# Optimization experiments

Measured on AMD Instinct MI355X. Metric: run time of the kernel, lower is better.

Reference implementation:

```python
import jax, jax.numpy as jnp
import numpy as np

EPS = 1e-8

def setup_inputs() -> dict:
    key = jax.random.key(0)
    k1, k2 = jax.random.split(key)
    B, C, H, W = 8, 21, 512, 512
    inp = jax.random.normal(k1, (B, C, H, W), dtype=jnp.float32)
    target = jax.random.uniform(k2, (B, C, H, W), dtype=jnp.float32)
    return {"input": inp, "target": target}

def reference(input, target):
    B, C, H, W = input.shape
    # argmax over class dim -> [B, H, W]
    pred = jnp.argmax(input, axis=1)
    # one-hot of prediction, flattened over spatial dims -> [B, HW, C]
    h = jax.nn.one_hot(pred.reshape(B, H * W), C, dtype=input.dtype)
    # target flattened over spatial dims -> [B, C, HW]
    y = target.reshape(B, C, H * W)
    # cm[b, i, j] = sum_n y[b, i, n] * h[b, n, j]  -> [B, C, C]
    cm = jnp.einsum('bin,bnj->bij', y, h)
    # row-normalize by target mass per class, then mean over batch -> [C, C]
    cm = cm / (jnp.sum(y, axis=2, keepdims=True) + EPS)
    return jnp.mean(cm, axis=0)
```

## Files before the change

kernel.cpp:

```cpp
#include <hip/hip_runtime.h>

#define NC 21
#define NB 8
#define HW (512*512)
#define EPS 1e-8f
#define NREP 8
#define NTILE 256
#define PSTRIDE 512

typedef float f32x4 __attribute__((ext_vector_type(4)));


template <bool PARTIAL>
__global__ __launch_bounds__(256) void cm_accum(const float* __restrict__ input,
                                                const float* __restrict__ target,
                                                float* __restrict__ cm ,
                                                float* __restrict__ partial ) {
    __shared__ float scm[NREP][NC * NC];
    const int t = threadIdx.x;
    for (int i = t; i < NREP * NC * NC; i += 256) ((float*)scm)[i] = 0.0f;
    __syncthreads();

    const int b    = blockIdx.x >> 8;
    const int tile = blockIdx.x & 255;
    const int q    = (tile << 8) + t;

    const f32x4* ip = (const f32x4*)(input  + (size_t)b * NC * HW);
    const f32x4* tp = (const f32x4*)(target + (size_t)b * NC * HW);
    const int plane4 = HW / 4;

    f32x4 v[NC];
    #pragma unroll
    for (int c = 0; c < NC; ++c) v[c] = __builtin_nontemporal_load(ip + c * plane4 + q);
    __builtin_amdgcn_sched_barrier(0);

    f32x4 m = v[0];
    int jx = 0, jy = 0, jz = 0, jw = 0;
    #pragma unroll
    for (int c = 1; c < NC; ++c) {
        if (v[c].x > m.x) { m.x = v[c].x; jx = c; }
        if (v[c].y > m.y) { m.y = v[c].y; jy = c; }
        if (v[c].z > m.z) { m.z = v[c].z; jz = c; }
        if (v[c].w > m.w) { m.w = v[c].w; jw = c; }
    }

    f32x4 y[NC];
    #pragma unroll
    for (int c = 0; c < NC; ++c) y[c] = __builtin_nontemporal_load(tp + c * plane4 + q);
    __builtin_amdgcn_sched_barrier(0);

    float* my = scm[t & (NREP - 1)];
    #pragma unroll
    for (int c = 0; c < NC; ++c) {
        const int row = c * NC;
        atomicAdd(&my[row + jx], y[c].x);
        atomicAdd(&my[row + jy], y[c].y);
        atomicAdd(&my[row + jz], y[c].z);
        atomicAdd(&my[row + jw], y[c].w);
    }
    __syncthreads();

    if (PARTIAL) {
        float* pout = partial + (size_t)blockIdx.x * PSTRIDE;
        for (int i = t; i < PSTRIDE; i += 256) {
            float s = 0.0f;
            if (i < NC * NC) {
                #pragma unroll
                for (int r = 0; r < NREP; ++r) s += scm[r][i];
            }
            pout[i] = s;
        }
    } else {
        for (int i = t; i < NC * NC; i += 256) {
            float s = 0.0f;
            #pragma unroll
            for (int r = 0; r < NREP; ++r) s += scm[r][i];
            atomicAdd(&cm[b * NC * NC + i], s);
        }
    }
}

__global__ __launch_bounds__(256) void cm_reduce(const float* __restrict__ partial,
                                                 float* __restrict__ cm) {
    const int b = blockIdx.x, t = threadIdx.x;
    const float* p = partial + (size_t)b * NTILE * PSTRIDE;
    float s0 = 0.0f, s1 = 0.0f;
    #pragma unroll 8
    for (int s = 0; s < NTILE; ++s) {
        s0 += p[(size_t)s * PSTRIDE + t];
        s1 += p[(size_t)s * PSTRIDE + t + 256];
    }
    cm[b * NC * NC + t] = s0;
    if (t + 256 < NC * NC) cm[b * NC * NC + t + 256] = s1;
}

__global__ __launch_bounds__(512) void cm_final(const float* __restrict__ cm,
                                                float* __restrict__ out) {
    __shared__ float rs[NB * NC];
    const int t = threadIdx.x;
    if (t < NB * NC) {
        const int b = t / NC, i = t % NC;
        float s = 0.0f;
        for (int j = 0; j < NC; ++j) s += cm[b * NC * NC + i * NC + j];
        rs[t] = s + EPS;
    }
    __syncthreads();
    if (t < NC * NC) {
        const int i = t / NC;
        float acc = 0.0f;
        for (int b = 0; b < NB; ++b) acc += cm[b * NC * NC + t] / rs[b * NC + i];
        out[t] = acc * (1.0f / NB);
    }
}

extern "C" void kernel_launch(void* const* d_in, const int* in_sizes, int n_in,
                              void* d_out, int out_size, void* d_ws, size_t ws_size,
                              hipStream_t stream) {
    const float* input  = (const float*)d_in[0];
    const float* target = (const float*)d_in[1];
    float* out = (float*)d_out;

    const size_t partial_floats = (size_t)NB * NTILE * PSTRIDE;
    const size_t need = (partial_floats + NB * NC * NC) * sizeof(float);

    if (ws_size >= need) {
        float* partial = (float*)d_ws;
        float* cm      = partial + partial_floats;
        cm_accum<true><<<NB * NTILE, 256, 0, stream>>>(input, target, cm, partial);
        cm_reduce<<<NB, 256, 0, stream>>>(partial, cm);
        cm_final<<<1, 512, 0, stream>>>(cm, out);
    } else {
        float* cm = (float*)d_ws;
        hipMemsetAsync(cm, 0, NB * NC * NC * sizeof(float), stream);
        cm_accum<false><<<NB * NTILE, 256, 0, stream>>>(input, target, cm, nullptr);
        cm_final<<<1, 512, 0, stream>>>(cm, out);
    }
}
```

Before: 514.8 us.

## Stream class planes with double-buffered loads, two float4 per thread, rotated start channel

```diff
diff --git a/kernel.cpp b/kernel.cpp
--- a/kernel.cpp
+++ b/kernel.cpp
@@ -1,68 +1,97 @@
 #include <hip/hip_runtime.h>
+#include <math.h>
 
 #define NC 21
 #define NB 8
 #define HW (512*512)
 #define EPS 1e-8f
 #define NREP 8
-#define NTILE 256
+#define TPB 256
+#define G4 2
+#define F4_PER_BLOCK (TPB * G4)
+#define TILES_PER_IMG (HW / 4 / F4_PER_BLOCK)
+#define NBLK (NB * TILES_PER_IMG)
 #define PSTRIDE 512
 
 typedef float f32x4 __attribute__((ext_vector_type(4)));
 
 
+#define UPD(val, cc, mm, jj) \
+    if ((val) > (mm) || ((val) == (mm) && (cc) < (jj))) { (mm) = (val); (jj) = (cc); }
+
 template <bool PARTIAL>
-__global__ __launch_bounds__(256) void cm_accum(const float* __restrict__ input,
+__global__ __launch_bounds__(TPB) void cm_accum(const float* __restrict__ input,
                                                 const float* __restrict__ target,
                                                 float* __restrict__ cm ,
                                                 float* __restrict__ partial ) {
     __shared__ float scm[NREP][NC * NC];
     const int t = threadIdx.x;
-    for (int i = t; i < NREP * NC * NC; i += 256) ((float*)scm)[i] = 0.0f;
+    for (int i = t; i < NREP * NC * NC; i += TPB) ((float*)scm)[i] = 0.0f;
     __syncthreads();
 
-    const int b    = blockIdx.x >> 8;
-    const int tile = blockIdx.x & 255;
-    const int q    = (tile << 8) + t;
+    const int bid  = blockIdx.x;
+    const int b    = bid / TILES_PER_IMG;
+    const int tile = bid % TILES_PER_IMG;
+    const int rot  = bid % NC;
 
     const f32x4* ip = (const f32x4*)(input  + (size_t)b * NC * HW);
     const f32x4* tp = (const f32x4*)(target + (size_t)b * NC * HW);
     const int plane4 = HW / 4;
+    const int q0 = tile * F4_PER_BLOCK + t;
 
-    f32x4 v[NC];
-    #pragma unroll
-    for (int c = 0; c < NC; ++c) v[c] = __builtin_nontemporal_load(ip + c * plane4 + q);
-    __builtin_amdgcn_sched_barrier(0);
+    f32x4 mA, mB;
+    mA.x = mA.y = mA.z = mA.w = -INFINITY;
+    mB.x = mB.y = mB.z = mB.w = -INFINITY;
+    int jAx = NC, jAy = NC, jAz = NC, jAw = NC;
+    int jBx = NC, jBy = NC, jBz = NC, jBw = NC;
 
-    f32x4 m = v[0];
-    int jx = 0, jy = 0, jz = 0, jw = 0;
-    #pragma unroll
-    for (int c = 1; c < NC; ++c) {
-        if (v[c].x > m.x) { m.x = v[c].x; jx = c; }
-        if (v[c].y > m.y) { m.y = v[c].y; jy = c; }
-        if (v[c].z > m.z) { m.z = v[c].z; jz = c; }
-        if (v[c].w > m.w) { m.w = v[c].w; jw = c; }
+    int c = rot;
+    f32x4 curA = __builtin_nontemporal_load(ip + (size_t)c * plane4 + q0);
+    f32x4 curB = __builtin_nontemporal_load(ip + (size_t)c * plane4 + q0 + TPB);
+    f32x4 nxtA = {}, nxtB = {};
+    for (int cc = 0; cc < NC; ++cc) {
+        const int cn = (c + 1 == NC) ? 0 : c + 1;
+        if (cc < NC - 1) {
+            nxtA = __builtin_nontemporal_load(ip + (size_t)cn * plane4 + q0);
+            nxtB = __builtin_nontemporal_load(ip + (size_t)cn * plane4 + q0 + TPB);
+        }
+        __builtin_amdgcn_sched_barrier(0);
+        UPD(curA.x, c, mA.x, jAx); UPD(curA.y, c, mA.y, jAy);
+        UPD(curA.z, c, mA.z, jAz); UPD(curA.w, c, mA.w, jAw);
+        UPD(curB.x, c, mB.x, jBx); UPD(curB.y, c, mB.y, jBy);
+        UPD(curB.z, c, mB.z, jBz); UPD(curB.w, c, mB.w, jBw);
+        curA = nxtA; curB = nxtB;
+        c = cn;
     }
 
-    f32x4 y[NC];
-    #pragma unroll
-    for (int c = 0; c < NC; ++c) y[c] = __builtin_nontemporal_load(tp + c * plane4 + q);
-    __builtin_amdgcn_sched_barrier(0);
-
     float* my = scm[t & (NREP - 1)];
-    #pragma unroll
-    for (int c = 0; c < NC; ++c) {
+    c = rot;
+    curA = __builtin_nontemporal_load(tp + (size_t)c * plane4 + q0);
+    curB = __builtin_nontemporal_load(tp + (size_t)c * plane4 + q0 + TPB);
+    for (int cc = 0; cc < NC; ++cc) {
+        const int cn = (c + 1 == NC) ? 0 : c + 1;
+        if (cc < NC - 1) {
+            nxtA = __builtin_nontemporal_load(tp + (size_t)cn * plane4 + q0);
+            nxtB = __builtin_nontemporal_load(tp + (size_t)cn * plane4 + q0 + TPB);
+        }
+        __builtin_amdgcn_sched_barrier(0);
         const int row = c * NC;
-        atomicAdd(&my[row + jx], y[c].x);
-        atomicAdd(&my[row + jy], y[c].y);
-        atomicAdd(&my[row + jz], y[c].z);
-        atomicAdd(&my[row + jw], y[c].w);
+        atomicAdd(&my[row + jAx], curA.x);
+        atomicAdd(&my[row + jAy], curA.y);
+        atomicAdd(&my[row + jAz], curA.z);
+        atomicAdd(&my[row + jAw], curA.w);
+        atomicAdd(&my[row + jBx], curB.x);
+        atomicAdd(&my[row + jBy], curB.y);
+        atomicAdd(&my[row + jBz], curB.z);
+        atomicAdd(&my[row + jBw], curB.w);
+        curA = nxtA; curB = nxtB;
+        c = cn;
     }
     __syncthreads();
 
     if (PARTIAL) {
-        float* pout = partial + (size_t)blockIdx.x * PSTRIDE;
-        for (int i = t; i < PSTRIDE; i += 256) {
+        float* pout = partial + (size_t)bid * PSTRIDE;
+        for (int i = t; i < PSTRIDE; i += TPB) {
             float s = 0.0f;
             if (i < NC * NC) {
                 #pragma unroll
@@ -71,7 +100,7 @@
             pout[i] = s;
         }
     } else {
-        for (int i = t; i < NC * NC; i += 256) {
+        for (int i = t; i < NC * NC; i += TPB) {
             float s = 0.0f;
             #pragma unroll
             for (int r = 0; r < NREP; ++r) s += scm[r][i];
@@ -83,10 +112,10 @@
 __global__ __launch_bounds__(256) void cm_reduce(const float* __restrict__ partial,
                                                  float* __restrict__ cm) {
     const int b = blockIdx.x, t = threadIdx.x;
-    const float* p = partial + (size_t)b * NTILE * PSTRIDE;
+    const float* p = partial + (size_t)b * TILES_PER_IMG * PSTRIDE;
     float s0 = 0.0f, s1 = 0.0f;
     #pragma unroll 8
-    for (int s = 0; s < NTILE; ++s) {
+    for (int s = 0; s < TILES_PER_IMG; ++s) {
         s0 += p[(size_t)s * PSTRIDE + t];
         s1 += p[(size_t)s * PSTRIDE + t + 256];
     }
@@ -120,19 +149,19 @@
     const float* target = (const float*)d_in[1];
     float* out = (float*)d_out;
 
-    const size_t partial_floats = (size_t)NB * NTILE * PSTRIDE;
+    const size_t partial_floats = (size_t)NBLK * PSTRIDE;
     const size_t need = (partial_floats + NB * NC * NC) * sizeof(float);
 
     if (ws_size >= need) {
         float* partial = (float*)d_ws;
         float* cm      = partial + partial_floats;
-        cm_accum<true><<<NB * NTILE, 256, 0, stream>>>(input, target, cm, partial);
+        cm_accum<true><<<NBLK, TPB, 0, stream>>>(input, target, cm, partial);
         cm_reduce<<<NB, 256, 0, stream>>>(partial, cm);
         cm_final<<<1, 512, 0, stream>>>(cm, out);
     } else {
         float* cm = (float*)d_ws;
         hipMemsetAsync(cm, 0, NB * NC * NC * sizeof(float), stream);
-        cm_accum<false><<<NB * NTILE, 256, 0, stream>>>(input, target, cm, nullptr);
+        cm_accum<false><<<NBLK, TPB, 0, stream>>>(input, target, cm, nullptr);
         cm_final<<<1, 512, 0, stream>>>(cm, out);
     }
 }
```

After: 516.4 us. No clear change (+0.3%).
